# Performance work log

Measured on AMD Instinct MI355X. Metric: run time of the kernel, lower is better.

## Reference

```python
import jax, jax.numpy as jnp
import numpy as np

B, N1, N2, DIM1, DIM2, DK = 4, 4096, 2048, 256, 256, 256


def setup_inputs() -> dict:
    key = jax.random.key(0)
    ks = jax.random.split(key, 8)
    s1 = 1.0 / np.sqrt(DIM2)  # torch Linear default init scale (uniform bound)
    s2 = 1.0 / np.sqrt(DIM1)
    return {
        "x1": jax.random.normal(ks[0], (B, N1, DIM1), jnp.float32),
        "x2": jax.random.normal(ks[1], (B, N2, DIM2), jnp.float32),
        "WQ": jax.random.uniform(ks[2], (DK, DIM2), jnp.float32, -s1, s1),
        "bQ": jax.random.uniform(ks[3], (DK,), jnp.float32, -s1, s1),
        "WK": jax.random.uniform(ks[4], (DK, DIM1), jnp.float32, -s2, s2),
        "bK": jax.random.uniform(ks[5], (DK,), jnp.float32, -s2, s2),
        "WV": jax.random.uniform(ks[6], (DK, DIM1), jnp.float32, -s2, s2),
        "bV": jax.random.uniform(ks[7], (DK,), jnp.float32, -s2, s2),
    }


def reference(x1, x2, WQ, bQ, WK, bK, WV, bV):
    # Projections (torch Linear: x @ W^T + b)
    Q = jnp.einsum('bnd,kd->bnk', x2, WQ) + bQ  # [B, N2, DK]
    K = jnp.einsum('bmd,kd->bmk', x1, WK) + bK  # [B, N1, DK]
    V = jnp.einsum('bmd,kd->bmk', x1, WV) + bV  # [B, N1, DK]

    QK = jnp.einsum('bnk,bmk->bnm', Q, K)                          # [B, N2, N1]
    P = (jnp.einsum('bnk,bmk->bnm', jnp.tanh(Q), jnp.tanh(K)) + 1.0) * 0.5
    scores = QK * P / jnp.sqrt(jnp.float32(DK))
    attn = jax.nn.softmax(scores, axis=-1)                         # [B, N2, N1]
    Q_hat = jnp.einsum('bnm,bmk->bnk', attn, V)                    # [B, N2, DK]
    return (Q, Q_hat, attn)
```

## Files before the change

kernel.cpp:

```cpp
#include <hip/hip_runtime.h>
#include <hip/hip_bf16.h>

typedef __bf16 bf16;
typedef __bf16 bf16x4 __attribute__((ext_vector_type(4)));
typedef __bf16 bf16x8 __attribute__((ext_vector_type(8)));
typedef float  f32x4  __attribute__((ext_vector_type(4)));

#define DEVI static __device__ __forceinline__

constexpr int NB = 4;
constexpr int N1 = 4096;
constexpr int N2 = 2048;
constexpr int D  = 256;

DEVI f32x4 mfma16(bf16x8 a, bf16x8 b, f32x4 c) {
  return __builtin_amdgcn_mfma_f32_16x16x32_bf16(a, b, c, 0, 0, 0);
}

typedef const __attribute__((address_space(1))) void* gas_t;
typedef __attribute__((address_space(3))) void* las_t;

DEVI void gload_lds16(const void* g, void* l) {
  __builtin_amdgcn_global_load_lds((gas_t)g, (las_t)l, 16, 0, 0);
}

DEVI void fence_sched() { __builtin_amdgcn_sched_barrier(0); }

__global__ __launch_bounds__(256)
void projQ_kernel(const float* __restrict__ A, const float* __restrict__ Bm,
                  const float* __restrict__ bias,
                  float* __restrict__ outF, bf16* __restrict__ out1,
                  bf16* __restrict__ out2)
{
  __shared__ bf16 Ah[128][64], Al[128][64];
  __shared__ bf16 Bh[64][64],  Bl[64][64];
  const int tid  = threadIdx.x;
  const int lane = tid & 63, wid = tid >> 6;
  const int wr = wid >> 1, wc = wid & 1;
  const int m0 = blockIdx.x * 128, n0 = blockIdx.y * 64;

  f32x4 acc[4][2];
#pragma unroll
  for (int i = 0; i < 4; ++i)
#pragma unroll
    for (int j = 0; j < 2; ++j) acc[i][j] = f32x4{0.f, 0.f, 0.f, 0.f};

  for (int kt = 0; kt < 4; ++kt) {
    const int k0 = kt * 64;
    if (kt) __syncthreads();
#pragma unroll
    for (int i = 0; i < 8; ++i) {
      int idx = i * 256 + tid;
      int r = idx >> 4, c4 = idx & 15;
      const float4 v = *(const float4*)(A + (size_t)(m0 + r) * D + k0 + c4 * 4);
      bf16x4 h, l;
      h[0] = (bf16)v.x; h[1] = (bf16)v.y; h[2] = (bf16)v.z; h[3] = (bf16)v.w;
      l[0] = (bf16)(v.x - (float)h[0]); l[1] = (bf16)(v.y - (float)h[1]);
      l[2] = (bf16)(v.z - (float)h[2]); l[3] = (bf16)(v.w - (float)h[3]);
      *(bf16x4*)&Ah[r][c4 * 4] = h;
      *(bf16x4*)&Al[r][c4 * 4] = l;
    }
#pragma unroll
    for (int i = 0; i < 4; ++i) {
      int idx = i * 256 + tid;
      int r = idx >> 4, c4 = idx & 15;
      const float4 v = *(const float4*)(Bm + (size_t)(n0 + r) * D + k0 + c4 * 4);
      bf16x4 h, l;
      h[0] = (bf16)v.x; h[1] = (bf16)v.y; h[2] = (bf16)v.z; h[3] = (bf16)v.w;
      l[0] = (bf16)(v.x - (float)h[0]); l[1] = (bf16)(v.y - (float)h[1]);
      l[2] = (bf16)(v.z - (float)h[2]); l[3] = (bf16)(v.w - (float)h[3]);
      *(bf16x4*)&Bh[r][c4 * 4] = h;
      *(bf16x4*)&Bl[r][c4 * 4] = l;
    }
    __syncthreads();
#pragma unroll
    for (int kc = 0; kc < 2; ++kc) {
      const int ko = kc * 32 + (lane >> 4) * 8;
      bf16x8 ah[4], al[4];
#pragma unroll
      for (int mf = 0; mf < 4; ++mf) {
        ah[mf] = *(bf16x8*)&Ah[wr * 64 + mf * 16 + (lane & 15)][ko];
        al[mf] = *(bf16x8*)&Al[wr * 64 + mf * 16 + (lane & 15)][ko];
      }
#pragma unroll
      for (int nf = 0; nf < 2; ++nf) {
        bf16x8 bh = *(bf16x8*)&Bh[wc * 32 + nf * 16 + (lane & 15)][ko];
        bf16x8 bl = *(bf16x8*)&Bl[wc * 32 + nf * 16 + (lane & 15)][ko];
#pragma unroll
        for (int mf = 0; mf < 4; ++mf) {
          acc[mf][nf] = mfma16(ah[mf], bh, acc[mf][nf]);
          acc[mf][nf] = mfma16(ah[mf], bl, acc[mf][nf]);
          acc[mf][nf] = mfma16(al[mf], bh, acc[mf][nf]);
        }
      }
    }
  }

#pragma unroll
  for (int nf = 0; nf < 2; ++nf) {
    const int col = n0 + wc * 32 + nf * 16 + (lane & 15);
    const float bcol = bias[col];
#pragma unroll
    for (int mf = 0; mf < 4; ++mf) {
#pragma unroll
      for (int r = 0; r < 4; ++r) {
        const int row = m0 + wr * 64 + mf * 16 + (lane >> 4) * 4 + r;
        float v = acc[mf][nf][r] + bcol;
        outF[(size_t)row * D + col] = v;
        out1[(size_t)row * D + col] = (bf16)v;
        out2[(size_t)row * D + col] = (bf16)tanhf(v);
      }
    }
  }
}

template<int MODE>
__global__ __launch_bounds__(256)
void proj_kernel(const float* __restrict__ A, const float* __restrict__ Bm,
                 const float* __restrict__ bias,
                 bf16* __restrict__ out1, bf16* __restrict__ out2)
{
  __shared__ bf16 As[128][64];
  __shared__ bf16 Bs[64][64];
  const int tid  = threadIdx.x;
  const int lane = tid & 63, wid = tid >> 6;
  const int wr = wid >> 1, wc = wid & 1;
  const int m0 = blockIdx.x * 128, n0 = blockIdx.y * 64;

  f32x4 acc[4][2];
#pragma unroll
  for (int i = 0; i < 4; ++i)
#pragma unroll
    for (int j = 0; j < 2; ++j) acc[i][j] = f32x4{0.f, 0.f, 0.f, 0.f};

  for (int kt = 0; kt < 4; ++kt) {
    const int k0 = kt * 64;
    if (kt) __syncthreads();
#pragma unroll
    for (int i = 0; i < 8; ++i) {
      int idx = i * 256 + tid;
      int r = idx >> 4, c4 = idx & 15;
      const float4 v = *(const float4*)(A + (size_t)(m0 + r) * D + k0 + c4 * 4);
      bf16x4 bv; bv[0] = (bf16)v.x; bv[1] = (bf16)v.y; bv[2] = (bf16)v.z; bv[3] = (bf16)v.w;
      *(bf16x4*)&As[r][c4 * 4] = bv;
    }
#pragma unroll
    for (int i = 0; i < 4; ++i) {
      int idx = i * 256 + tid;
      int r = idx >> 4, c4 = idx & 15;
      const float4 v = *(const float4*)(Bm + (size_t)(n0 + r) * D + k0 + c4 * 4);
      bf16x4 bv; bv[0] = (bf16)v.x; bv[1] = (bf16)v.y; bv[2] = (bf16)v.z; bv[3] = (bf16)v.w;
      *(bf16x4*)&Bs[r][c4 * 4] = bv;
    }
    __syncthreads();
#pragma unroll
    for (int kc = 0; kc < 2; ++kc) {
      const int ko = kc * 32 + (lane >> 4) * 8;
      bf16x8 a[4];
#pragma unroll
      for (int mf = 0; mf < 4; ++mf)
        a[mf] = *(bf16x8*)&As[wr * 64 + mf * 16 + (lane & 15)][ko];
#pragma unroll
      for (int nf = 0; nf < 2; ++nf) {
        bf16x8 bb = *(bf16x8*)&Bs[wc * 32 + nf * 16 + (lane & 15)][ko];
#pragma unroll
        for (int mf = 0; mf < 4; ++mf) acc[mf][nf] = mfma16(a[mf], bb, acc[mf][nf]);
      }
    }
  }

#pragma unroll
  for (int nf = 0; nf < 2; ++nf) {
    const int col = n0 + wc * 32 + nf * 16 + (lane & 15);
    float bcol = 0.f;
    if constexpr (MODE == 1) bcol = bias[col];
#pragma unroll
    for (int mf = 0; mf < 4; ++mf) {
#pragma unroll
      for (int r = 0; r < 4; ++r) {
        const int row = m0 + wr * 64 + mf * 16 + (lane >> 4) * 4 + r;
        float v = acc[mf][nf][r];
        if constexpr (MODE == 1) {
          v += bcol;
          out1[(size_t)row * D + col] = (bf16)v;
          out2[(size_t)row * D + col] = (bf16)tanhf(v);
        } else {
          v += bias[row];
          out1[(size_t)(col >> 12) * (D * N1) + (size_t)row * N1 + (col & 4095)] = (bf16)v;
        }
      }
    }
  }
}

__global__ __launch_bounds__(512, 4)
void scores_kernel(const bf16* __restrict__ Qb, const bf16* __restrict__ tQb,
                   const bf16* __restrict__ Kb, const bf16* __restrict__ tKb,
                   bf16* __restrict__ E, float* __restrict__ partials)
{
  __shared__ bf16 SM[2][4][128][32];
  __shared__ float rowpart[128][4];
  const int tid = threadIdx.x, lane = tid & 63, wid = tid >> 6;
  const int wr = wid >> 2;
  const int wc = wid & 3;
  const int lo16 = lane & 15, hi = lane >> 4;
  const int mt = blockIdx.x, nt = blockIdx.y, b = blockIdx.z;
  const int RQ = b * N2 + nt * 128;
  const int RK = b * N1 + mt * 128;

  f32x4 accS[4][2], accP[4][2];
#pragma unroll
  for (int i = 0; i < 4; ++i)
#pragma unroll
    for (int j = 0; j < 2; ++j) {
      accS[i][j] = f32x4{0.f, 0.f, 0.f, 0.f};
      accP[i][j] = f32x4{0.f, 0.f, 0.f, 0.f};
    }

  const int srow = tid >> 2;
  const int scol = (tid & 3) * 8;

  auto stage = [&](int kt, int buf) {
    const int col = kt * 32 + scol;
    char* base = (char*)&SM[buf][0][0][0] + tid * 16;
    gload_lds16(Qb  + (size_t)(RQ + srow) * D + col, base);
    gload_lds16(tQb + (size_t)(RQ + srow) * D + col, base + 8192);
    gload_lds16(Kb  + (size_t)(RK + srow) * D + col, base + 16384);
    gload_lds16(tKb + (size_t)(RK + srow) * D + col, base + 24576);
  };

  auto cpt = [&](int buf) {
    const int ko = hi * 8;
    bf16x8 aS[4], aT[4];
#pragma unroll
    for (int mf = 0; mf < 4; ++mf) {
      aS[mf] = *(bf16x8*)&SM[buf][0][wr * 64 + mf * 16 + lo16][ko];
      aT[mf] = *(bf16x8*)&SM[buf][1][wr * 64 + mf * 16 + lo16][ko];
    }
#pragma unroll
    for (int nf = 0; nf < 2; ++nf) {
      bf16x8 bS = *(bf16x8*)&SM[buf][2][wc * 32 + nf * 16 + lo16][ko];
      bf16x8 bT = *(bf16x8*)&SM[buf][3][wc * 32 + nf * 16 + lo16][ko];
#pragma unroll
      for (int mf = 0; mf < 4; ++mf) {
        accS[mf][nf] = mfma16(aS[mf], bS, accS[mf][nf]);
        accP[mf][nf] = mfma16(aT[mf], bT, accP[mf][nf]);
      }
    }
  };

  stage(0, 0);
  fence_sched();
  int cur = 0;
#pragma unroll
  for (int kt = 0; kt < 8; ++kt) {
    if (kt < 7) {
      stage(kt + 1, cur ^ 1);
      fence_sched();
      asm volatile("s_waitcnt vmcnt(4)\n\ts_barrier" ::: "memory");
    } else {
      asm volatile("s_waitcnt vmcnt(0)\n\ts_barrier" ::: "memory");
    }
    cpt(cur);
    asm volatile("s_barrier" ::: "memory");
    cur ^= 1;
  }

#pragma unroll
  for (int mf = 0; mf < 4; ++mf) {
    f32x4 rs = f32x4{0.f, 0.f, 0.f, 0.f};
#pragma unroll
    for (int nf = 0; nf < 2; ++nf) {
      const int m_g = mt * 128 + wc * 32 + nf * 16 + lo16;
#pragma unroll
      for (int r = 0; r < 4; ++r) {
        const int n_g = b * N2 + nt * 128 + wr * 64 + mf * 16 + hi * 4 + r;
        float s = accS[mf][nf][r] * (accP[mf][nf][r] + 1.0f) * 0.03125f;
        float e = __expf(s);
        E[(size_t)n_g * N1 + m_g] = (bf16)e;
        rs[r] += e;
      }
    }
#pragma unroll
    for (int r = 0; r < 4; ++r) {
      float v = rs[r];
      v += __shfl_xor(v, 1); v += __shfl_xor(v, 2);
      v += __shfl_xor(v, 4); v += __shfl_xor(v, 8);
      if (lo16 == 0)
        rowpart[wr * 64 + mf * 16 + hi * 4 + r][wc] = v;
    }
  }
  __syncthreads();
  if (tid < 128) {
    float p = rowpart[tid][0] + rowpart[tid][1] + rowpart[tid][2] + rowpart[tid][3];
    partials[(size_t)(b * N2 + nt * 128 + tid) * 32 + mt] = p;
  }
}

__global__ __launch_bounds__(512, 4)
void qhat_kernel(const bf16* __restrict__ E, const bf16* __restrict__ Vt,
                 const float* __restrict__ partials,
                 float* __restrict__ attn, bf16* __restrict__ partQ)
{
  __shared__ bf16 As[2][64][64];
  __shared__ bf16 Bs[2][256][64];
  const int tid = threadIdx.x, lane = tid & 63, wid = tid >> 6;
  const int lo16 = lane & 15, hi = lane >> 4, sw = lane & 7;
  const int n0 = blockIdx.x * 64;
  const int mh = blockIdx.y;
  const int b  = blockIdx.z;
  const int mq = mh * 1024;
  const int arow = tid >> 3;
  const int mo   = (tid & 7) * 8;
  const size_t rglob = (size_t)b * N2 + n0 + arow;

  float s = 0.f;
  {
    const float* pr = partials + rglob * 32;
#pragma unroll
    for (int j = 0; j < 32; ++j) s += pr[j];
  }
  const float inv = 1.0f / s;

  const bf16* erow  = E    + rglob * N1 + mq;
  float*      aorow = attn + rglob * N1 + mq;
  const bf16* vbase = Vt + (size_t)b * (D * N1) + mq;
  const int awcol = ((tid & 7) ^ (arow & 7)) << 3;

  f32x4 acc[4][2];
#pragma unroll
  for (int i = 0; i < 4; ++i)
#pragma unroll
    for (int j = 0; j < 2; ++j) acc[i][j] = f32x4{0.f, 0.f, 0.f, 0.f};

  auto loadE = [&](int ms) -> bf16x8 {
    return *(const bf16x8*)(erow + ms * 64 + mo);
  };
  auto stageB = [&](int ms, int buf) {
#pragma unroll
    for (int i = 0; i < 4; ++i) {
      const int c = i * 512 + tid;
      const int row = c >> 3;
      gload_lds16(vbase + (size_t)row * N1 + ms * 64 + (((c & 7) ^ (row & 7)) << 3),
                  (char*)&Bs[buf][0][0] + c * 16);
    }
  };
  auto procA = [&](int ms, int buf, bf16x8 e) {
    float v[8]; bf16x8 svv;
#pragma unroll
    for (int j = 0; j < 8; ++j) { v[j] = (float)e[j] * inv; svv[j] = (bf16)v[j]; }
    float4 w0 = {v[0], v[1], v[2], v[3]};
    float4 w1 = {v[4], v[5], v[6], v[7]};
    *(float4*)(aorow + ms * 64 + mo)     = w0;
    *(float4*)(aorow + ms * 64 + mo + 4) = w1;
    *(bf16x8*)((char*)&As[buf][arow][0] + awcol * 2) = svv;
  };
  auto cptq = [&](int buf) {
#pragma unroll
    for (int kc = 0; kc < 2; ++kc) {
      const int ko = (((kc * 4 + hi) ^ sw) << 3);
      bf16x8 a[4];
#pragma unroll
      for (int mf = 0; mf < 4; ++mf)
        a[mf] = *(bf16x8*)&As[buf][mf * 16 + lo16][ko];
#pragma unroll
      for (int nf = 0; nf < 2; ++nf) {
        bf16x8 bb = *(bf16x8*)&Bs[buf][wid * 32 + nf * 16 + lo16][ko];
#pragma unroll
        for (int mf = 0; mf < 4; ++mf) acc[mf][nf] = mfma16(a[mf], bb, acc[mf][nf]);
      }
    }
  };

  bf16x8 ev[2];
  ev[0] = loadE(0);
  procA(0, 0, ev[0]);
  fence_sched();
  stageB(0, 0);
  fence_sched();
  ev[1] = loadE(1);
  fence_sched();

  int cur = 0;
#pragma unroll
  for (int ms = 0; ms < 16; ++ms) {
    if (ms < 15) {
      procA(ms + 1, cur ^ 1, ev[(ms + 1) & 1]);
      fence_sched();
      stageB(ms + 1, cur ^ 1);
      fence_sched();
      if (ms < 14) { ev[ms & 1] = loadE(ms + 2); fence_sched(); }
    }
    if (ms < 14)
      asm volatile("s_waitcnt vmcnt(7) lgkmcnt(0)\n\ts_barrier" ::: "memory");
    else if (ms == 14)
      asm volatile("s_waitcnt vmcnt(6) lgkmcnt(0)\n\ts_barrier" ::: "memory");
    else
      asm volatile("s_waitcnt vmcnt(0) lgkmcnt(0)\n\ts_barrier" ::: "memory");
    cptq(cur);
    asm volatile("s_barrier" ::: "memory");
    cur ^= 1;
  }

#pragma unroll
  for (int mf = 0; mf < 4; ++mf)
#pragma unroll
    for (int nf = 0; nf < 2; ++nf)
#pragma unroll
      for (int r = 0; r < 4; ++r) {
        const int n  = n0 + mf * 16 + hi * 4 + r;
        const int dk = wid * 32 + nf * 16 + lo16;
        partQ[((size_t)(mh * NB + b) * N2 + n) * D + dk] = (bf16)acc[mf][nf][r];
      }
}

__global__ __launch_bounds__(256)
void reduceQ_kernel(const bf16* __restrict__ P, float* __restrict__ Qhat)
{
  const size_t i = ((size_t)blockIdx.x * 256 + threadIdx.x) * 8;
  const size_t S = (size_t)NB * N2 * D;
  bf16x8 p0 = *(const bf16x8*)(P + i);
  bf16x8 p1 = *(const bf16x8*)(P + S + i);
  bf16x8 p2 = *(const bf16x8*)(P + 2 * S + i);
  bf16x8 p3 = *(const bf16x8*)(P + 3 * S + i);
  float o[8];
#pragma unroll
  for (int j = 0; j < 8; ++j)
    o[j] = ((float)p0[j] + (float)p1[j]) + ((float)p2[j] + (float)p3[j]);
  float4 w0 = {o[0], o[1], o[2], o[3]};
  float4 w1 = {o[4], o[5], o[6], o[7]};
  *(float4*)(Qhat + i)     = w0;
  *(float4*)(Qhat + i + 4) = w1;
}

extern "C" void kernel_launch(void* const* d_in, const int* in_sizes, int n_in,
                              void* d_out, int out_size, void* d_ws, size_t ws_size,
                              hipStream_t stream)
{
  const float* x1 = (const float*)d_in[0];
  const float* x2 = (const float*)d_in[1];
  const float* WQ = (const float*)d_in[2];
  const float* bQ = (const float*)d_in[3];
  const float* WK = (const float*)d_in[4];
  const float* bK = (const float*)d_in[5];
  const float* WV = (const float*)d_in[6];
  const float* bV = (const float*)d_in[7];

  float* out  = (float*)d_out;
  float* Qf   = out;
  float* Qhat = out + 2097152;
  float* attn = out + 4194304;

  char* ws = (char*)d_ws;
  bf16* Qb   = (bf16*)(ws + (0ull  << 20));
  bf16* tQb  = (bf16*)(ws + (4ull  << 20));
  bf16* Kb   = (bf16*)(ws + (8ull  << 20));
  bf16* tKb  = (bf16*)(ws + (16ull << 20));
  bf16* Vt   = (bf16*)(ws + (24ull << 20));
  bf16* E    = (bf16*)(ws + (32ull << 20));
  float* partials = (float*)(ws + (96ull << 20));
  bf16*  partQ    = (bf16*)(ws + (100ull << 20));

  projQ_kernel    <<<dim3(64, 4),   256, 0, stream>>>(x2, WQ, bQ, Qf, Qb, tQb);
  proj_kernel<1>  <<<dim3(128, 4),  256, 0, stream>>>(x1, WK, bK, Kb, tKb);
  proj_kernel<2>  <<<dim3(2, 256),  256, 0, stream>>>(WV, x1, bV, Vt, nullptr);
  scores_kernel   <<<dim3(32, 16, 4), 512, 0, stream>>>(Qb, tQb, Kb, tKb, E, partials);
  qhat_kernel     <<<dim3(32, 4, 4), 512, 0, stream>>>(E, Vt, partials, attn, partQ);
  reduceQ_kernel  <<<1024, 256, 0, stream>>>(partQ, Qhat);
}
```

Before: 178.2 us.

## Drop split-K in qhat kernel and swizzle scores LDS tiles

The qhat kernel no longer splits the N1 reduction into four quarters that write bf16 partials for a separate reduce kernel. Each block now owns 32 query rows across all of N1 (64 steps, not unrolled) and writes fp32 Qhat directly. This removes the partial round-trip and one launch, and accumulates in fp32 without bf16 rounding of partials. The cost is fewer blocks (256 instead of 512), a longer serial loop, and Vt tiles reloaded once per 32 rows instead of per 64. Separately, the scores kernel applies an XOR swizzle to its LDS staging and fragment reads to cut bank conflicts.

```diff
diff --git a/kernel.cpp b/kernel.cpp
--- a/kernel.cpp
+++ b/kernel.cpp
@@ -218,7 +218,7 @@
     }
 
   const int srow = tid >> 2;
-  const int scol = (tid & 3) * 8;
+  const int scol = ((tid & 3) ^ ((srow >> 1) & 3)) << 3;
 
   auto stage = [&](int kt, int buf) {
     const int col = kt * 32 + scol;
@@ -230,17 +230,20 @@
   };
 
   auto cpt = [&](int buf) {
-    const int ko = hi * 8;
     bf16x8 aS[4], aT[4];
 #pragma unroll
     for (int mf = 0; mf < 4; ++mf) {
-      aS[mf] = *(bf16x8*)&SM[buf][0][wr * 64 + mf * 16 + lo16][ko];
-      aT[mf] = *(bf16x8*)&SM[buf][1][wr * 64 + mf * 16 + lo16][ko];
+      const int row = wr * 64 + mf * 16 + lo16;
+      const int ko = (hi ^ ((row >> 1) & 3)) << 3;
+      aS[mf] = *(bf16x8*)&SM[buf][0][row][ko];
+      aT[mf] = *(bf16x8*)&SM[buf][1][row][ko];
     }
 #pragma unroll
     for (int nf = 0; nf < 2; ++nf) {
-      bf16x8 bS = *(bf16x8*)&SM[buf][2][wc * 32 + nf * 16 + lo16][ko];
-      bf16x8 bT = *(bf16x8*)&SM[buf][3][wc * 32 + nf * 16 + lo16][ko];
+      const int row = wc * 32 + nf * 16 + lo16;
+      const int ko = (hi ^ ((row >> 1) & 3)) << 3;
+      bf16x8 bS = *(bf16x8*)&SM[buf][2][row][ko];
+      bf16x8 bT = *(bf16x8*)&SM[buf][3][row][ko];
 #pragma unroll
       for (int mf = 0; mf < 4; ++mf) {
         accS[mf][nf] = mfma16(aS[mf], bS, accS[mf][nf]);
@@ -297,21 +300,20 @@
   }
 }
 
-__global__ __launch_bounds__(512, 4)
+__global__ __launch_bounds__(512)
 void qhat_kernel(const bf16* __restrict__ E, const bf16* __restrict__ Vt,
                  const float* __restrict__ partials,
-                 float* __restrict__ attn, bf16* __restrict__ partQ)
+                 float* __restrict__ attn, float* __restrict__ Qhat)
 {
-  __shared__ bf16 As[2][64][64];
+  __shared__ bf16 As[2][32][64];
   __shared__ bf16 Bs[2][256][64];
   const int tid = threadIdx.x, lane = tid & 63, wid = tid >> 6;
-  const int lo16 = lane & 15, hi = lane >> 4, sw = lane & 7;
-  const int n0 = blockIdx.x * 64;
-  const int mh = blockIdx.y;
-  const int b  = blockIdx.z;
-  const int mq = mh * 1024;
-  const int arow = tid >> 3;
-  const int mo   = (tid & 7) * 8;
+  const int lo16 = lane & 15, hi = lane >> 4;
+  const int n0 = blockIdx.x * 32;
+  const int b  = blockIdx.y;
+  const int arow  = tid >> 4;
+  const int mquad = tid & 15;
+  const int mo    = mquad * 4;
   const size_t rglob = (size_t)b * N2 + n0 + arow;
 
   float s = 0.f;
@@ -322,57 +324,57 @@
   }
   const float inv = 1.0f / s;
 
-  const bf16* erow  = E    + rglob * N1 + mq;
-  float*      aorow = attn + rglob * N1 + mq;
-  const bf16* vbase = Vt + (size_t)b * (D * N1) + mq;
-  const int awcol = ((tid & 7) ^ (arow & 7)) << 3;
-
-  f32x4 acc[4][2];
-#pragma unroll
-  for (int i = 0; i < 4; ++i)
+  const bf16* erow  = E    + rglob * N1;
+  float*      aorow = attn + rglob * N1;
+  const bf16* vbase = Vt + (size_t)b * (D * N1);
+  const int awbyte = arow * 128 + (((mquad >> 1) ^ (arow & 7)) << 4) + (mquad & 1) * 8;
+
+  f32x4 acc[2][2];
+#pragma unroll
+  for (int i = 0; i < 2; ++i)
 #pragma unroll
     for (int j = 0; j < 2; ++j) acc[i][j] = f32x4{0.f, 0.f, 0.f, 0.f};
 
-  auto loadE = [&](int ms) -> bf16x8 {
-    return *(const bf16x8*)(erow + ms * 64 + mo);
+  auto loadE = [&](int ms) -> bf16x4 {
+    return *(const bf16x4*)(erow + ms * 64 + mo);
   };
   auto stageB = [&](int ms, int buf) {
 #pragma unroll
     for (int i = 0; i < 4; ++i) {
       const int c = i * 512 + tid;
       const int row = c >> 3;
-      gload_lds16(vbase + (size_t)row * N1 + ms * 64 + (((c & 7) ^ (row & 7)) << 3),
+      gload_lds16(vbase + (size_t)row * N1 + ms * 64 + ((((c & 7) ^ (row & 7))) << 3),
                   (char*)&Bs[buf][0][0] + c * 16);
     }
   };
-  auto procA = [&](int ms, int buf, bf16x8 e) {
-    float v[8]; bf16x8 svv;
-#pragma unroll
-    for (int j = 0; j < 8; ++j) { v[j] = (float)e[j] * inv; svv[j] = (bf16)v[j]; }
+  auto procA = [&](int ms, int buf, bf16x4 e) {
+    float v[4]; bf16x4 svv;
+#pragma unroll
+    for (int j = 0; j < 4; ++j) { v[j] = (float)e[j] * inv; svv[j] = (bf16)v[j]; }
     float4 w0 = {v[0], v[1], v[2], v[3]};
-    float4 w1 = {v[4], v[5], v[6], v[7]};
-    *(float4*)(aorow + ms * 64 + mo)     = w0;
-    *(float4*)(aorow + ms * 64 + mo + 4) = w1;
-    *(bf16x8*)((char*)&As[buf][arow][0] + awcol * 2) = svv;
+    *(float4*)(aorow + ms * 64 + mo) = w0;
+    *(bf16x4*)((char*)&As[buf][0][0] + awbyte) = svv;
   };
   auto cptq = [&](int buf) {
 #pragma unroll
     for (int kc = 0; kc < 2; ++kc) {
-      const int ko = (((kc * 4 + hi) ^ sw) << 3);
-      bf16x8 a[4];
-#pragma unroll
-      for (int mf = 0; mf < 4; ++mf)
-        a[mf] = *(bf16x8*)&As[buf][mf * 16 + lo16][ko];
+      bf16x8 a[2];
+#pragma unroll
+      for (int mf = 0; mf < 2; ++mf) {
+        const int row = mf * 16 + lo16;
+        a[mf] = *(bf16x8*)&As[buf][row][(((kc * 4 + hi) ^ (row & 7))) << 3];
+      }
 #pragma unroll
       for (int nf = 0; nf < 2; ++nf) {
-        bf16x8 bb = *(bf16x8*)&Bs[buf][wid * 32 + nf * 16 + lo16][ko];
-#pragma unroll
-        for (int mf = 0; mf < 4; ++mf) acc[mf][nf] = mfma16(a[mf], bb, acc[mf][nf]);
-      }
-    }
-  };
-
-  bf16x8 ev[2];
+        const int row = wid * 32 + nf * 16 + lo16;
+        bf16x8 bb = *(bf16x8*)&Bs[buf][row][(((kc * 4 + hi) ^ (row & 7))) << 3];
+#pragma unroll
+        for (int mf = 0; mf < 2; ++mf) acc[mf][nf] = mfma16(a[mf], bb, acc[mf][nf]);
+      }
+    }
+  };
+
+  bf16x4 ev[2];
   ev[0] = loadE(0);
   procA(0, 0, ev[0]);
   fence_sched();
@@ -382,19 +384,18 @@
   fence_sched();
 
   int cur = 0;
-#pragma unroll
-  for (int ms = 0; ms < 16; ++ms) {
-    if (ms < 15) {
+  for (int ms = 0; ms < 64; ++ms) {
+    if (ms < 63) {
       procA(ms + 1, cur ^ 1, ev[(ms + 1) & 1]);
       fence_sched();
       stageB(ms + 1, cur ^ 1);
       fence_sched();
-      if (ms < 14) { ev[ms & 1] = loadE(ms + 2); fence_sched(); }
-    }
-    if (ms < 14)
-      asm volatile("s_waitcnt vmcnt(7) lgkmcnt(0)\n\ts_barrier" ::: "memory");
-    else if (ms == 14)
+      if (ms < 62) { ev[ms & 1] = loadE(ms + 2); fence_sched(); }
+    }
+    if (ms < 62)
       asm volatile("s_waitcnt vmcnt(6) lgkmcnt(0)\n\ts_barrier" ::: "memory");
+    else if (ms == 62)
+      asm volatile("s_waitcnt vmcnt(5) lgkmcnt(0)\n\ts_barrier" ::: "memory");
     else
       asm volatile("s_waitcnt vmcnt(0) lgkmcnt(0)\n\ts_barrier" ::: "memory");
     cptq(cur);
@@ -403,34 +404,15 @@
   }
 
 #pragma unroll
-  for (int mf = 0; mf < 4; ++mf)
+  for (int mf = 0; mf < 2; ++mf)
 #pragma unroll
     for (int nf = 0; nf < 2; ++nf)
 #pragma unroll
       for (int r = 0; r < 4; ++r) {
         const int n  = n0 + mf * 16 + hi * 4 + r;
         const int dk = wid * 32 + nf * 16 + lo16;
-        partQ[((size_t)(mh * NB + b) * N2 + n) * D + dk] = (bf16)acc[mf][nf][r];
-      }
-}
-
-__global__ __launch_bounds__(256)
-void reduceQ_kernel(const bf16* __restrict__ P, float* __restrict__ Qhat)
-{
-  const size_t i = ((size_t)blockIdx.x * 256 + threadIdx.x) * 8;
-  const size_t S = (size_t)NB * N2 * D;
-  bf16x8 p0 = *(const bf16x8*)(P + i);
-  bf16x8 p1 = *(const bf16x8*)(P + S + i);
-  bf16x8 p2 = *(const bf16x8*)(P + 2 * S + i);
-  bf16x8 p3 = *(const bf16x8*)(P + 3 * S + i);
-  float o[8];
-#pragma unroll
-  for (int j = 0; j < 8; ++j)
-    o[j] = ((float)p0[j] + (float)p1[j]) + ((float)p2[j] + (float)p3[j]);
-  float4 w0 = {o[0], o[1], o[2], o[3]};
-  float4 w1 = {o[4], o[5], o[6], o[7]};
-  *(float4*)(Qhat + i)     = w0;
-  *(float4*)(Qhat + i + 4) = w1;
+        Qhat[((size_t)b * N2 + n) * D + dk] = acc[mf][nf][r];
+      }
 }
 
 extern "C" void kernel_launch(void* const* d_in, const int* in_sizes, int n_in,
@@ -459,12 +441,10 @@
   bf16* Vt   = (bf16*)(ws + (24ull << 20));
   bf16* E    = (bf16*)(ws + (32ull << 20));
   float* partials = (float*)(ws + (96ull << 20));
-  bf16*  partQ    = (bf16*)(ws + (100ull << 20));
 
   projQ_kernel    <<<dim3(64, 4),   256, 0, stream>>>(x2, WQ, bQ, Qf, Qb, tQb);
   proj_kernel<1>  <<<dim3(128, 4),  256, 0, stream>>>(x1, WK, bK, Kb, tKb);
   proj_kernel<2>  <<<dim3(2, 256),  256, 0, stream>>>(WV, x1, bV, Vt, nullptr);
   scores_kernel   <<<dim3(32, 16, 4), 512, 0, stream>>>(Qb, tQb, Kb, tKb, E, partials);
-  qhat_kernel     <<<dim3(32, 4, 4), 512, 0, stream>>>(E, Vt, partials, attn, partQ);
-  reduceQ_kernel  <<<1024, 256, 0, stream>>>(partQ, Qhat);
-}
+  qhat_kernel     <<<dim3(64, 4), 512, 0, stream>>>(E, Vt, partials, attn, Qhat);
+}
```

After: 217.5 us. 1.22x slower.
